# Kernel tuning notes

Measured on AMD Instinct MI355X. Metric: run time of the kernel, lower is better.

Reference implementation:

```python
import jax, jax.numpy as jnp
import numpy as np

D_MODEL, H, KV, HD = 2048, 32, 8, 64  # head_dim = 64, RoPE half-dim = 32
B, L = 2, 2048
EPS = 1e-06


def apply_rope(t, cos, sin):
    # t: [b,l,h,hd]; cos/sin: [1,l,1,hd//2] (broadcast over batch and heads)
    dim = t.shape[-1] // 2
    cos = cos[..., :dim]
    sin = sin[..., :dim]
    x1, x2 = t[..., :dim], t[..., dim:]
    return jnp.concatenate([x1 * cos - x2 * sin, x2 * cos + x1 * sin], axis=-1)


def setup_inputs() -> dict:
    key = jax.random.key(0)
    ks = jax.random.split(key, 5)
    x = jax.random.normal(ks[0], (B, L, D_MODEL), dtype=jnp.float32)
    # true rotary tables, theta=10000
    half = HD // 2
    inv_freq = 1.0 / (10000.0 ** (jnp.arange(half, dtype=jnp.float32) / half))
    ang = jnp.arange(L, dtype=jnp.float32)[:, None] * inv_freq[None, :]  # [L, half]
    cos = jnp.cos(ang)[None, :, None, :]  # [1,L,1,half]
    sin = jnp.sin(ang)[None, :, None, :]
    s = 0.02
    Wq = jax.random.normal(ks[1], (D_MODEL, D_MODEL), dtype=jnp.float32) * s
    Wk = jax.random.normal(ks[2], (D_MODEL, KV * HD), dtype=jnp.float32) * s
    Wv = jax.random.normal(ks[3], (D_MODEL, KV * HD), dtype=jnp.float32) * s
    Wo = jax.random.normal(ks[4], (D_MODEL, D_MODEL), dtype=jnp.float32) * s
    return {"x": x, "cos": cos, "sin": sin, "Wq": Wq, "Wk": Wk, "Wv": Wv, "Wo": Wo}


def reference(x, cos, sin, Wq, Wk, Wv, Wo):
    b, l, _ = x.shape
    q = (x @ Wq).reshape(b, l, H, HD)
    k = (x @ Wk).reshape(b, l, KV, HD)
    v = (x @ Wv).reshape(b, l, KV, HD)
    q = apply_rope(q, cos, sin)
    k = apply_rope(k, cos[:, :, :KV, :], sin[:, :, :KV, :])
    # QK RMS-norm (qk_norm=True path), done in fp32
    q32 = q.astype(jnp.float32)
    k32 = k.astype(jnp.float32)
    q = (q32 * jax.lax.rsqrt(jnp.mean(jnp.square(q32), axis=-1, keepdims=True) + EPS)).astype(q.dtype)
    k = (k32 * jax.lax.rsqrt(jnp.mean(jnp.square(k32), axis=-1, keepdims=True) + EPS)).astype(k.dtype)
    # GQA: repeat KV heads to match Q heads
    g = H // KV
    k = jnp.repeat(k, g, axis=2)
    v = jnp.repeat(v, g, axis=2)
    scale = jax.lax.rsqrt(jnp.float32(HD))
    scores = jnp.einsum('blhd,bmhd->bhlm', q, k) * scale  # [b,H,L,L]
    causal = jnp.tril(jnp.ones((l, l), dtype=jnp.bool_))[None, None]
    scores = jnp.where(causal, scores, jnp.full_like(scores, -10000.0))
    attn = jax.nn.softmax(scores.astype(jnp.float32), axis=-1).astype(v.dtype)
    out = jnp.einsum('bhql,blhd->bqhd', attn, v).reshape(b, l, D_MODEL)
    return out @ Wo
```

## Files before the change

### kernel.cpp

```cpp
#include <hip/hip_runtime.h>
#include <hip/hip_bf16.h>
#include <cstdint>
#include <cstddef>

#define D_MODEL 2048
#define NH 32
#define NKV 8
#define HD 64
#define BB 2
#define LL 2048
#define EPS 1e-6f
#define MM (BB * LL)
#define QS 3072
#define KO 2048
#define VO 2560
#define QSCALE 0.18033688f
#define SM_BIAS 11.5415603f

typedef __hip_bfloat16 bf16;
typedef short bf16x8 __attribute__((ext_vector_type(8)));
typedef short s16x4 __attribute__((ext_vector_type(4)));
typedef float f32x4 __attribute__((ext_vector_type(4)));

__device__ inline float4 ld_bf4u(const unsigned short* p) {
  const ushort4 u = *(const ushort4*)p;
  float4 r;
  r.x = __uint_as_float(((unsigned)u.x) << 16);
  r.y = __uint_as_float(((unsigned)u.y) << 16);
  r.z = __uint_as_float(((unsigned)u.z) << 16);
  r.w = __uint_as_float(((unsigned)u.w) << 16);
  return r;
}
__device__ inline float4 ld4_rt(const void* p, size_t i, bool f32) {
  if (f32) return *(const float4*)((const float*)p + i);
  return ld_bf4u((const unsigned short*)p + i);
}
__device__ inline float ld1_rt(const void* p, size_t i, bool f32) {
  if (f32) return ((const float*)p)[i];
  unsigned short u = ((const unsigned short*)p)[i];
  return __uint_as_float(((unsigned)u) << 16);
}
__device__ inline unsigned short f2bf(float f) {
  bf16 h = __float2bfloat16(f);
  return *reinterpret_cast<unsigned short*>(&h);
}
__device__ inline float bfu2f(unsigned short u) {
  return __uint_as_float(((unsigned)u) << 16);
}
__device__ inline void store1(float* p, float v) { *p = v; }
__device__ inline void store1(unsigned short* p, float v) { *p = f2bf(v); }

__device__ inline void glds16(const unsigned short* g, unsigned short* l) {
  __builtin_amdgcn_global_load_lds(
      (const __attribute__((address_space(1))) unsigned int*)g,
      (__attribute__((address_space(3))) unsigned int*)l, 16, 0, 0);
}

__global__ __launch_bounds__(256) void detect_all(
    const unsigned short* p0, const unsigned short* p1, const unsigned short* p2,
    const unsigned short* p3, const unsigned short* p4, const unsigned short* p5,
    const unsigned short* p6, int* __restrict__ flags) {
  const unsigned short* ptrs[7] = {p0, p1, p2, p3, p4, p5, p6};
  const int b = blockIdx.x;
  const uint4* p = (const uint4*)ptrs[b];
  __shared__ int found;
  if (threadIdx.x == 0) found = 0;
  __syncthreads();
  int loc = 0;
#pragma unroll
  for (int it = 0; it < 16; ++it) {
    uint4 v = p[it * 256 + threadIdx.x];
    unsigned wds[4] = {v.x, v.y, v.z, v.w};
#pragma unroll
    for (int q = 0; q < 4; ++q) {
      unsigned lo = wds[q] & 0xFFFFu, hi = wds[q] >> 16;
      if (((lo >> 7) & 0xFFu) == 0xFFu || ((hi >> 7) & 0xFFu) == 0xFFu) loc = 1;
    }
  }
  if (loc) atomicOr(&found, 1);
  __syncthreads();
  if (threadIdx.x == 0) flags[b] = found;
}

__global__ __launch_bounds__(256) void cvt_bf16(const void* __restrict__ src,
                                                unsigned short* __restrict__ dst,
                                                int n4, const int* __restrict__ flags, int idx) {
  const bool f32 = flags[idx] != 0;
  int i = blockIdx.x * 256 + threadIdx.x;
  if (i < n4) {
    float4 v = ld4_rt(src, (size_t)i * 4, f32);
    ushort4 o;
    o.x = f2bf(v.x); o.y = f2bf(v.y); o.z = f2bf(v.z); o.w = f2bf(v.w);
    *(ushort4*)&dst[(size_t)i * 4] = o;
  }
}

__global__ __launch_bounds__(256) void transpose_all(
    const void* __restrict__ Wq, const void* __restrict__ Wk,
    const void* __restrict__ Wv, const void* __restrict__ Wo,
    unsigned short* __restrict__ WqkvT, unsigned short* __restrict__ WoT,
    const int* __restrict__ flags) {
  const int z = blockIdx.z;
  const void* srcs[4] = {Wq, Wk, Wv, Wo};
  unsigned short* dsts[4] = {WqkvT, WqkvT + (size_t)KO * 2048, WqkvT + (size_t)VO * 2048, WoT};
  const int Ns[4] = {2048, 512, 512, 2048};
  const int N = Ns[z];
  if (blockIdx.x * 64 >= N) return;
  const void* src = srcs[z];
  unsigned short* dst = dsts[z];
  const bool f32 = flags[3 + z] != 0;
  const int K = 2048;
  __shared__ unsigned short tile[64][65];
  const int t = threadIdx.x;
  const int n0 = blockIdx.x * 64, k0 = blockIdx.y * 64;
  const int cr = t >> 4, cc = (t & 15) * 4;
#pragma unroll
  for (int rr = 0; rr < 4; ++rr) {
    int row = rr * 16 + cr;
    float4 v = ld4_rt(src, (size_t)(k0 + row) * N + n0 + cc, f32);
    tile[row][cc + 0] = f2bf(v.x);
    tile[row][cc + 1] = f2bf(v.y);
    tile[row][cc + 2] = f2bf(v.z);
    tile[row][cc + 3] = f2bf(v.w);
  }
  __syncthreads();
#pragma unroll
  for (int rr = 0; rr < 4; ++rr) {
    int nrow = rr * 16 + cr;
    ushort4 o;
    o.x = tile[cc + 0][nrow];
    o.y = tile[cc + 1][nrow];
    o.z = tile[cc + 2][nrow];
    o.w = tile[cc + 3][nrow];
    *(ushort4*)&dst[(size_t)(n0 + nrow) * K + k0 + cc] = o;
  }
}

__global__ __launch_bounds__(256) void v_to_vt(const unsigned short* __restrict__ qkv,
                                               unsigned short* __restrict__ vt) {
  __shared__ unsigned short tile[64][72];
  const int t = threadIdx.x;
  const int l0 = blockIdx.x * 64;
  const int bk = blockIdx.y;
  const int r = t >> 2, c16 = (t & 3) * 16;
  const int b = bk >> 3, kvh = bk & 7;
  const unsigned short* src = &qkv[(size_t)(b * LL + l0 + r) * QS + VO + kvh * 64 + c16];
  *(uint4*)&tile[r][c16] = *(const uint4*)&src[0];
  *(uint4*)&tile[r][c16 + 8] = *(const uint4*)&src[8];
  __syncthreads();
  unsigned short u[16];
#pragma unroll
  for (int j = 0; j < 16; ++j) u[j] = tile[c16 + j][r];
  unsigned short* dst = &vt[((size_t)bk * 64 + r) * LL + l0 + c16];
  *(uint4*)&dst[0] = *(uint4*)&u[0];
  *(uint4*)&dst[8] = *(uint4*)&u[8];
}

template <typename CT, int FUSE>
__global__ __launch_bounds__(256) void gemm_mfma(const unsigned short* __restrict__ A,
                                                 const unsigned short* __restrict__ Bt,
                                                 CT* __restrict__ C,
                                                 int M, int N, int K, int lda,
                                                 const void* __restrict__ cosp,
                                                 const void* __restrict__ sinp,
                                                 const int* __restrict__ flags) {
  __shared__ __align__(16) unsigned short As[3][128 * 32];
  __shared__ __align__(16) unsigned short Bs[3][128 * 32];
  const int t = threadIdx.x;
  const int lane = t & 63, w = t >> 6;
  const int wm = (w >> 1) * 64, wn = (w & 1) * 64;
  const int g = lane >> 4, m16 = lane & 15;
  const int nwg = gridDim.x * gridDim.y;
  const int orig = blockIdx.y * gridDim.x + blockIdx.x;
  const int swz = (orig & 7) * (nwg >> 3) + (orig >> 3);
  const int m0 = (swz / gridDim.x) * 128, n0 = (swz % gridDim.x) * 128;
  const unsigned short* gA = &A[(size_t)(m0 + (t >> 2)) * lda + (t & 3) * 8];
  const unsigned short* gB = &Bt[(size_t)(n0 + (t >> 2)) * K + (t & 3) * 8];
  const int l8 = t * 8;
  f32x4 acc[4][4] = {};
  const int T = K >> 5;

#define STAGE(k0_, buf_)                                        \
  do {                                                          \
    glds16(gA + (k0_), &As[buf_][l8]);                          \
    glds16(gA + (size_t)64 * lda + (k0_), &As[buf_][l8 + 2048]);\
    glds16(gB + (k0_), &Bs[buf_][l8]);                          \
    glds16(gB + (size_t)64 * K + (k0_), &Bs[buf_][l8 + 2048]);  \
  } while (0)

  STAGE(0, 0);
  STAGE(32, 1);
  asm volatile("s_waitcnt vmcnt(4)" ::: "memory");
  __builtin_amdgcn_s_barrier();

  int buf = 0;
  for (int tt = 0; tt < T; ++tt) {
    const int k0 = tt << 5;
    if (tt + 2 < T) {
      int nb = buf + 2; if (nb >= 3) nb -= 3;
      STAGE(k0 + 64, nb);
    }
    bf16x8 af[4], bfr[4];
#pragma unroll
    for (int i = 0; i < 4; ++i) af[i] = *(const bf16x8*)&As[buf][(wm + i * 16 + m16) * 32 + g * 8];
#pragma unroll
    for (int j = 0; j < 4; ++j) bfr[j] = *(const bf16x8*)&Bs[buf][(wn + j * 16 + m16) * 32 + g * 8];
#pragma unroll
    for (int i = 0; i < 4; ++i)
#pragma unroll
      for (int j = 0; j < 4; ++j)
        acc[i][j] = __builtin_amdgcn_mfma_f32_16x16x32_bf16(af[i], bfr[j], acc[i][j], 0, 0, 0);
    if (tt + 1 < T) {
      if (tt + 2 < T) asm volatile("s_waitcnt vmcnt(4)" ::: "memory");
      else            asm volatile("s_waitcnt vmcnt(0)" ::: "memory");
      __builtin_amdgcn_s_barrier();
    }
    ++buf; if (buf >= 3) buf = 0;
  }
#undef STAGE

  if constexpr (FUSE) {
    const int colbase = n0 + wn;
    if (colbase < VO) {
      const bool cf = flags[1] != 0, sf = flags[2] != 0;
      const float post = (colbase < KO) ? QSCALE : 1.0f;
#pragma unroll
      for (int i = 0; i < 4; ++i)
#pragma unroll
        for (int r = 0; r < 4; ++r) {
          const int row = m0 + wm + i * 16 + g * 4 + r;
          const int l = row & (LL - 1);
          const float c0 = ld1_rt(cosp, l * 32 + m16, cf);
          const float c1 = ld1_rt(cosp, l * 32 + 16 + m16, cf);
          const float s0 = ld1_rt(sinp, l * 32 + m16, sf);
          const float s1 = ld1_rt(sinp, l * 32 + 16 + m16, sf);
          const float x0 = acc[i][0][r], x1 = acc[i][1][r];
          const float x2 = acc[i][2][r], x3 = acc[i][3][r];
          const float r0 = x0 * c0 - x2 * s0;
          const float r1 = x1 * c1 - x3 * s1;
          const float r2 = x2 * c0 + x0 * s0;
          const float r3 = x3 * c1 + x1 * s1;
          float ss = r0 * r0 + r1 * r1 + r2 * r2 + r3 * r3;
#pragma unroll
          for (int off = 1; off < 16; off <<= 1) ss += __shfl_xor(ss, off);
          const float sc = rsqrtf(ss * (1.0f / HD) + EPS) * post;
          CT* cr = &C[(size_t)row * N + colbase + m16];
          store1(cr + 0, r0 * sc);
          store1(cr + 16, r1 * sc);
          store1(cr + 32, r2 * sc);
          store1(cr + 48, r3 * sc);
        }
      return;
    }
  }
#pragma unroll
  for (int i = 0; i < 4; ++i)
#pragma unroll
    for (int j = 0; j < 4; ++j)
#pragma unroll
      for (int r = 0; r < 4; ++r) {
        int row = m0 + wm + i * 16 + g * 4 + r;
        int col = n0 + wn + j * 16 + m16;
        store1(&C[(size_t)row * N + col], acc[i][j][r]);
      }
}

__global__ __launch_bounds__(256) void attn_mfma(unsigned short* __restrict__ qkv,
                                                 const unsigned short* __restrict__ vt) {
  __shared__ __align__(16) unsigned short Ks[2][64 * 64];
  __shared__ __align__(16) unsigned short Vs[2][64 * 64];
  __shared__ __align__(16) unsigned short Pt[4][64 * 16];
  const int t = threadIdx.x, lane = t & 63, w = t >> 6;
  const int g = lane >> 4, m16 = lane & 15;
  const int h = blockIdx.x, b = blockIdx.y;
  const int qt = (LL / 64 - 1) - blockIdx.z;
  const int kvh = h >> 2;
  const int q0 = qt * 64, qr0 = q0 + w * 16;

  bf16x8 qf0, qf1;
  {
    const unsigned short* qrow = &qkv[(size_t)(b * LL + qr0 + m16) * QS + h * 64 + g * 8];
    qf0 = *(const bf16x8*)&qrow[0];
    qf1 = *(const bf16x8*)&qrow[32];
  }
  f32x4 Oacc[4] = {};
  float lrow[4] = {0.f, 0.f, 0.f, 0.f};

  const int lr = lane >> 3;
  const int lc = (lane & 7) ^ lr;
  const unsigned short* gK = &qkv[(size_t)(b * LL) * QS + KO + kvh * 64 + lc * 8];
  const unsigned short* gV = &vt[((size_t)(b * NKV + kvh) * 64 + w * 16 + lr) * LL + lc * 8];
  const int dbase = w * 1024 + lane * 8;
  const int nIter = q0 / 64 + 1;

#pragma unroll
  for (int c = 0; c < 2; ++c) {
    glds16(gK + (size_t)(w * 16 + c * 8 + lr) * QS, &Ks[0][dbase + c * 512]);
    glds16(gV + (size_t)c * 8 * LL, &Vs[0][dbase + c * 512]);
  }
  __syncthreads();

  const int sw8 = (m16 & 7) * 8;
  for (int it = 0; it < nIter; ++it) {
    const int j0 = it * 64;
    const int cur = it & 1;
    if (it + 1 < nIter) {
      const int nj = j0 + 64;
#pragma unroll
      for (int c = 0; c < 2; ++c) {
        glds16(gK + (size_t)(nj + w * 16 + c * 8 + lr) * QS, &Ks[cur ^ 1][dbase + c * 512]);
        glds16(gV + (size_t)c * 8 * LL + nj, &Vs[cur ^ 1][dbase + c * 512]);
      }
    }
    const unsigned short* KsB = Ks[cur];
    const unsigned short* VsB = Vs[cur];

    f32x4 S[4];
#pragma unroll
    for (int jt = 0; jt < 4; ++jt) {
      const int rb = (jt * 16 + m16) * 64;
      bf16x8 kf0 = *(const bf16x8*)&KsB[rb + ((g * 8) ^ sw8)];
      bf16x8 kf1 = *(const bf16x8*)&KsB[rb + (((g + 4) * 8) ^ sw8)];
      f32x4 z = {0.f, 0.f, 0.f, 0.f};
      z = __builtin_amdgcn_mfma_f32_16x16x32_bf16(qf0, kf0, z, 0, 0, 0);
      S[jt] = __builtin_amdgcn_mfma_f32_16x16x32_bf16(qf1, kf1, z, 0, 0, 0);
    }
    if (j0 == q0) {
#pragma unroll
      for (int jt = 0; jt < 4; ++jt)
#pragma unroll
        for (int r = 0; r < 4; ++r) {
          int col = q0 + jt * 16 + m16;
          int row = qr0 + g * 4 + r;
          float p = exp2f(S[jt][r] - SM_BIAS);
          p = (col <= row) ? p : 0.f;
          S[jt][r] = p;
          lrow[r] += p;
        }
    } else {
#pragma unroll
      for (int jt = 0; jt < 4; ++jt)
#pragma unroll
        for (int r = 0; r < 4; ++r) {
          float p = exp2f(S[jt][r] - SM_BIAS);
          S[jt][r] = p;
          lrow[r] += p;
        }
    }
#pragma unroll
    for (int jt = 0; jt < 4; ++jt) {
      ushort4 pw;
      pw.x = f2bf(S[jt][0]); pw.y = f2bf(S[jt][1]);
      pw.z = f2bf(S[jt][2]); pw.w = f2bf(S[jt][3]);
      *(ushort4*)&Pt[w][(jt * 16 + m16) * 16 + g * 4] = pw;
    }
    s16x4 a0, a1, b0, b1;
    {
      __attribute__((address_space(3))) unsigned short* p3 =
          (__attribute__((address_space(3))) unsigned short*)&Pt[w][g * 128 + m16 * 4];
      unsigned paddr = (unsigned)(size_t)p3;
      asm volatile(
          "s_waitcnt lgkmcnt(0)\n\t"
          "ds_read_b64_tr_b16 %0, %4\n\t"
          "ds_read_b64_tr_b16 %1, %4 offset:128\n\t"
          "ds_read_b64_tr_b16 %2, %4 offset:1024\n\t"
          "ds_read_b64_tr_b16 %3, %4 offset:1152\n\t"
          "s_waitcnt lgkmcnt(0)"
          : "=&v"(a0), "=&v"(a1), "=&v"(b0), "=&v"(b1)
          : "v"(paddr)
          : "memory");
      __builtin_amdgcn_sched_barrier(0);
    }
    bf16x8 pf0 = __builtin_shufflevector(a0, a1, 0, 1, 2, 3, 4, 5, 6, 7);
    bf16x8 pf1 = __builtin_shufflevector(b0, b1, 0, 1, 2, 3, 4, 5, 6, 7);
#pragma unroll
    for (int dt = 0; dt < 4; ++dt) {
      const int rb = (dt * 16 + m16) * 64;
      bf16x8 vf0 = *(const bf16x8*)&VsB[rb + ((g * 8) ^ sw8)];
      bf16x8 vf1 = *(const bf16x8*)&VsB[rb + (((g + 4) * 8) ^ sw8)];
      Oacc[dt] = __builtin_amdgcn_mfma_f32_16x16x32_bf16(pf0, vf0, Oacc[dt], 0, 0, 0);
      Oacc[dt] = __builtin_amdgcn_mfma_f32_16x16x32_bf16(pf1, vf1, Oacc[dt], 0, 0, 0);
    }
    __syncthreads();
  }
  float inv[4];
#pragma unroll
  for (int r = 0; r < 4; ++r) {
#pragma unroll
    for (int off = 1; off < 16; off <<= 1) lrow[r] += __shfl_xor(lrow[r], off);
    inv[r] = 1.0f / lrow[r];
  }
#pragma unroll
  for (int dt = 0; dt < 4; ++dt)
#pragma unroll
    for (int r = 0; r < 4; ++r) {
      int row = qr0 + g * 4 + r;
      qkv[(size_t)(b * LL + row) * QS + h * 64 + dt * 16 + m16] = f2bf(Oacc[dt][r] * inv[r]);
    }
}

extern "C" void kernel_launch(void* const* d_in, const int* in_sizes, int n_in,
                              void* d_out, int out_size, void* d_ws, size_t ws_size,
                              hipStream_t stream) {
  const void* x = d_in[0];
  const void* cosp = d_in[1];
  const void* sinp = d_in[2];
  const void* Wq = d_in[3];
  const void* Wk = d_in[4];
  const void* Wv = d_in[5];
  const void* Wo = d_in[6];
  float* out = (float*)d_out;

  char* w0 = (char*)d_ws;
  int* flags = (int*)w0;
  unsigned short* xb = (unsigned short*)(w0 + 256);
  unsigned short* qkvb = xb + (size_t)MM * 2048;
  unsigned short* WqkvT = qkvb + (size_t)MM * QS;
  unsigned short* WoT = WqkvT + (size_t)QS * 2048;
  unsigned short* vt = WoT + (size_t)2048 * 2048;

  detect_all<<<7, 256, 0, stream>>>(
      (const unsigned short*)x, (const unsigned short*)cosp, (const unsigned short*)sinp,
      (const unsigned short*)Wq, (const unsigned short*)Wk, (const unsigned short*)Wv,
      (const unsigned short*)Wo, flags);
  cvt_bf16<<<MM * 2048 / 4 / 256, 256, 0, stream>>>(x, xb, MM * 2048 / 4, flags, 0);
  transpose_all<<<dim3(32, 32, 4), 256, 0, stream>>>(Wq, Wk, Wv, Wo, WqkvT, WoT, flags);
  gemm_mfma<unsigned short, 1><<<dim3(QS / 128, MM / 128), 256, 0, stream>>>(
      xb, WqkvT, qkvb, MM, QS, 2048, 2048, cosp, sinp, flags);
  v_to_vt<<<dim3(LL / 64, BB * NKV), 256, 0, stream>>>(qkvb, vt);
  attn_mfma<<<dim3(NH, BB, LL / 64), 256, 0, stream>>>(qkvb, vt);
  gemm_mfma<float, 0><<<dim3(2048 / 128, MM / 128), 256, 0, stream>>>(
      qkvb, WoT, out, MM, 2048, 2048, QS, nullptr, nullptr, nullptr);
}
```

Baseline: 327.5 us.

## Fuse V transpose into QKV GEMM epilogue, swizzle GEMM LDS, use fast exp2

The QKV GEMM epilogue now writes V tiles directly in transposed layout to the vt buffer, so the separate v_to_vt kernel launch and its extra pass over V are removed. The GEMM also XOR-swizzles the 8-element column chunk on both the global-to-LDS load and the LDS fragment reads to reduce bank conflicts. The attention softmax uses the hardware exp2 builtin instead of exp2f, which may be slightly less accurate. V is no longer written into qkvb, which is fine only if nothing else reads that region; the attention kernel appears to read V from vt.

Measured after the change: 317.1 us. 1.03x faster.

```diff
diff --git a/kernel.cpp b/kernel.cpp
--- a/kernel.cpp
+++ b/kernel.cpp
@@ -136,26 +136,6 @@
   }
 }
 
-__global__ __launch_bounds__(256) void v_to_vt(const unsigned short* __restrict__ qkv,
-                                               unsigned short* __restrict__ vt) {
-  __shared__ unsigned short tile[64][72];
-  const int t = threadIdx.x;
-  const int l0 = blockIdx.x * 64;
-  const int bk = blockIdx.y;
-  const int r = t >> 2, c16 = (t & 3) * 16;
-  const int b = bk >> 3, kvh = bk & 7;
-  const unsigned short* src = &qkv[(size_t)(b * LL + l0 + r) * QS + VO + kvh * 64 + c16];
-  *(uint4*)&tile[r][c16] = *(const uint4*)&src[0];
-  *(uint4*)&tile[r][c16 + 8] = *(const uint4*)&src[8];
-  __syncthreads();
-  unsigned short u[16];
-#pragma unroll
-  for (int j = 0; j < 16; ++j) u[j] = tile[c16 + j][r];
-  unsigned short* dst = &vt[((size_t)bk * 64 + r) * LL + l0 + c16];
-  *(uint4*)&dst[0] = *(uint4*)&u[0];
-  *(uint4*)&dst[8] = *(uint4*)&u[8];
-}
-
 template <typename CT, int FUSE>
 __global__ __launch_bounds__(256) void gemm_mfma(const unsigned short* __restrict__ A,
                                                  const unsigned short* __restrict__ Bt,
@@ -163,7 +143,8 @@
                                                  int M, int N, int K, int lda,
                                                  const void* __restrict__ cosp,
                                                  const void* __restrict__ sinp,
-                                                 const int* __restrict__ flags) {
+                                                 const int* __restrict__ flags,
+                                                 unsigned short* __restrict__ vt) {
   __shared__ __align__(16) unsigned short As[3][128 * 32];
   __shared__ __align__(16) unsigned short Bs[3][128 * 32];
   const int t = threadIdx.x;
@@ -174,9 +155,11 @@
   const int orig = blockIdx.y * gridDim.x + blockIdx.x;
   const int swz = (orig & 7) * (nwg >> 3) + (orig >> 3);
   const int m0 = (swz / gridDim.x) * 128, n0 = (swz % gridDim.x) * 128;
-  const unsigned short* gA = &A[(size_t)(m0 + (t >> 2)) * lda + (t & 3) * 8];
-  const unsigned short* gB = &Bt[(size_t)(n0 + (t >> 2)) * K + (t & 3) * 8];
+  const int csw = (t & 3) ^ ((t >> 3) & 3);
+  const unsigned short* gA = &A[(size_t)(m0 + (t >> 2)) * lda + csw * 8];
+  const unsigned short* gB = &Bt[(size_t)(n0 + (t >> 2)) * K + csw * 8];
   const int l8 = t * 8;
+  const int cs8 = (g ^ ((m16 >> 1) & 3)) * 8;
   f32x4 acc[4][4] = {};
   const int T = K >> 5;
 
@@ -202,9 +185,9 @@
     }
     bf16x8 af[4], bfr[4];
 #pragma unroll
-    for (int i = 0; i < 4; ++i) af[i] = *(const bf16x8*)&As[buf][(wm + i * 16 + m16) * 32 + g * 8];
-#pragma unroll
-    for (int j = 0; j < 4; ++j) bfr[j] = *(const bf16x8*)&Bs[buf][(wn + j * 16 + m16) * 32 + g * 8];
+    for (int i = 0; i < 4; ++i) af[i] = *(const bf16x8*)&As[buf][(wm + i * 16 + m16) * 32 + cs8];
+#pragma unroll
+    for (int j = 0; j < 4; ++j) bfr[j] = *(const bf16x8*)&Bs[buf][(wn + j * 16 + m16) * 32 + cs8];
 #pragma unroll
     for (int i = 0; i < 4; ++i)
 #pragma unroll
@@ -250,8 +233,22 @@
           store1(cr + 32, r2 * sc);
           store1(cr + 48, r3 * sc);
         }
-      return;
-    }
+    } else {
+      const int bb = (m0 + wm) >> 11;
+      const int lb = (m0 + wm) & (LL - 1);
+      const int kvh = (colbase - VO) >> 6;
+      unsigned short* vb = vt + (size_t)(bb * NKV + kvh) * 64 * LL;
+#pragma unroll
+      for (int j = 0; j < 4; ++j)
+#pragma unroll
+        for (int i = 0; i < 4; ++i) {
+          ushort4 pw;
+          pw.x = f2bf(acc[i][j][0]); pw.y = f2bf(acc[i][j][1]);
+          pw.z = f2bf(acc[i][j][2]); pw.w = f2bf(acc[i][j][3]);
+          *(ushort4*)&vb[(size_t)(j * 16 + m16) * LL + lb + i * 16 + g * 4] = pw;
+        }
+    }
+    return;
   }
 #pragma unroll
   for (int i = 0; i < 4; ++i)
@@ -332,7 +329,7 @@
         for (int r = 0; r < 4; ++r) {
           int col = q0 + jt * 16 + m16;
           int row = qr0 + g * 4 + r;
-          float p = exp2f(S[jt][r] - SM_BIAS);
+          float p = __builtin_amdgcn_exp2f(S[jt][r] - SM_BIAS);
           p = (col <= row) ? p : 0.f;
           S[jt][r] = p;
           lrow[r] += p;
@@ -342,7 +339,7 @@
       for (int jt = 0; jt < 4; ++jt)
 #pragma unroll
         for (int r = 0; r < 4; ++r) {
-          float p = exp2f(S[jt][r] - SM_BIAS);
+          float p = __builtin_amdgcn_exp2f(S[jt][r] - SM_BIAS);
           S[jt][r] = p;
           lrow[r] += p;
         }
@@ -426,9 +423,8 @@
   cvt_bf16<<<MM * 2048 / 4 / 256, 256, 0, stream>>>(x, xb, MM * 2048 / 4, flags, 0);
   transpose_all<<<dim3(32, 32, 4), 256, 0, stream>>>(Wq, Wk, Wv, Wo, WqkvT, WoT, flags);
   gemm_mfma<unsigned short, 1><<<dim3(QS / 128, MM / 128), 256, 0, stream>>>(
-      xb, WqkvT, qkvb, MM, QS, 2048, 2048, cosp, sinp, flags);
-  v_to_vt<<<dim3(LL / 64, BB * NKV), 256, 0, stream>>>(qkvb, vt);
+      xb, WqkvT, qkvb, MM, QS, 2048, 2048, cosp, sinp, flags, vt);
   attn_mfma<<<dim3(NH, BB, LL / 64), 256, 0, stream>>>(qkvb, vt);
   gemm_mfma<float, 0><<<dim3(2048 / 128, MM / 128), 256, 0, stream>>>(
-      qkvb, WoT, out, MM, 2048, 2048, QS, nullptr, nullptr, nullptr);
-}
+      qkvb, WoT, out, MM, 2048, 2048, QS, nullptr, nullptr, nullptr, nullptr);
+}
```
